# Optimization experiments

Measured on AMD Instinct MI355X. Metric: run time of the kernel, lower is better.

The kernel has to match this reference:

```python
import jax, jax.numpy as jnp
import numpy as np

B = 4            # batch
L = 4096         # max_len
D_MODEL = 1024   # qkv_dim == out_features
H = 16           # num_heads
SEG = 64         # max_seg_len
HD = D_MODEL // H          # head_dim = 64
NSEG = L // SEG            # num segments = 64
NEG = -1e10


def setup_inputs() -> dict:
    key = jax.random.key(0)
    k0, k1, k2, k3, k4 = jax.random.split(key, 5)
    scale = 1.0 / np.sqrt(D_MODEL).astype(np.float32)
    x = jax.random.normal(k0, (B, L, D_MODEL), jnp.float32)
    wq = jax.random.normal(k1, (D_MODEL, H, HD), jnp.float32) * scale
    wk = jax.random.normal(k2, (D_MODEL, H, HD), jnp.float32) * scale
    wv = jax.random.normal(k3, (D_MODEL, H, HD), jnp.float32) * scale
    wo = jax.random.normal(k4, (H, HD, D_MODEL), jnp.float32) * scale
    return {"input_qkv": x, "wq": wq, "wk": wk, "wv": wv, "wo": wo}


def reference(input_qkv, wq, wk, wv, wo):
    inv_sqrt_hd = 1.0 / np.sqrt(HD).astype(np.float32)
    # QKV projections; query pre-scaled by 1/sqrt(head_dim) as in get_qkv
    q = jnp.einsum('bld,dhf->blhf', input_qkv, wq) * inv_sqrt_hd
    k = jnp.einsum('bld,dhf->blhf', input_qkv, wk)
    v = jnp.einsum('bld,dhf->blhf', input_qkv, wv)

    cq = q.reshape(B * NSEG, SEG, H, HD)
    ck = k.reshape(B * NSEG, SEG, H, HD)
    cv = v.reshape(B * NSEG, SEG, H, HD)

    # Pooled per-segment query attends over its own segment's keys/values.
    # Original: merged_query = max(cq)*sqrt(HD), then flax dot_product_attention
    # rescales by 1/sqrt(HD) -> the two scalings cancel, so use max(cq) directly.
    mq = jnp.max(cq, axis=1, keepdims=True)                    # [B*NSEG, 1, H, HD]
    s_logits = jnp.einsum('bqhd,bkhd->bhqk', mq, ck)
    s_w = jax.nn.softmax(s_logits, axis=-1)
    s = jnp.einsum('bhqk,bkhd->bqhd', s_w, cv)                  # [B*NSEG, 1, H, HD]
    span_val = s.reshape(B, NSEG, H, HD)
    span_key = jnp.max(ck, axis=1).reshape(B, NSEG, H, HD)

    # Local causal attention logits within each segment
    causal = jnp.tril(jnp.ones((SEG, SEG), bool))
    local_bias = jnp.where(causal, 0.0, NEG).astype(jnp.float32)[None, :, None, :]
    local_logits = jnp.einsum('bqhd,bkhd->bqhk', cq, ck) + local_bias
    local_logits = local_logits.reshape(B, L, H, SEG)

    # Cross-segment logits: each token attends to strictly earlier segment summaries
    seg_id = jnp.arange(NSEG)
    prev_bias = jnp.where(seg_id[:, None] > seg_id[None, :], 0.0, NEG).astype(jnp.float32)
    prev_bias = jnp.repeat(prev_bias, SEG, axis=0)[None, :, None, :]  # [1, L, 1, NSEG]
    prev_logits = jnp.einsum('bqhd,bkhd->bqhk', q, span_key) + prev_bias

    # Joint softmax over [local keys | previous-segment summaries]
    joint = jnp.concatenate([local_logits, prev_logits], axis=-1)   # [B, L, H, SEG+NSEG]
    w = jax.nn.softmax(joint, axis=-1)
    local_att = w[..., :SEG].reshape(B * NSEG, SEG, H, SEG)
    prev_att = w[..., SEG:]

    local_merged = jnp.einsum('bqhk,bkhd->bqhd', local_att, cv).reshape(B, L, H, HD)
    prev_merged = jnp.einsum('bqhk,bkhd->bqhd', prev_att, span_val)

    return jnp.einsum('blhd,hdf->blf', local_merged + prev_merged, wo)
```

## Files before the change

kernel.cpp:

```cpp
#include <hip/hip_runtime.h>

#define BB    4
#define LL    4096
#define DM    1024
#define HH    16
#define SEGC  64
#define HDC   64
#define NSEGC 64
#define NEGV  -1.0e10f

typedef __bf16 bf16x8 __attribute__((ext_vector_type(8)));
typedef float  f32x4  __attribute__((ext_vector_type(4)));

__device__ __forceinline__ float bf2f(unsigned short s) {
  union { unsigned int u; float f; } x; x.u = ((unsigned int)s) << 16; return x.f;
}
__device__ __forceinline__ unsigned short f2bf(float f) {
  union { float f; unsigned int u; } x; x.f = f;
  unsigned int u = x.u;
  return (unsigned short)((u + 0x7fffu + ((u >> 16) & 1u)) >> 16);
}

__device__ __forceinline__ void gl2lds16(const unsigned short* g, unsigned short* l) {
  __builtin_amdgcn_global_load_lds(
      (const __attribute__((address_space(1))) unsigned int*)g,
      (__attribute__((address_space(3))) unsigned int*)l,
      16, 0, 0);
}

__device__ __forceinline__ void g2lds16(unsigned short* dst, const unsigned short* src) {
  int4 a = *(const int4*)(src);
  int4 b = *(const int4*)(src + 8);
  unsigned int* d = (unsigned int*)dst;
  const unsigned int* pa = (const unsigned int*)&a;
  const unsigned int* pb = (const unsigned int*)&b;
  d[0]=pa[0]; d[1]=pa[1]; d[2]=pa[2]; d[3]=pa[3];
  d[4]=pb[0]; d[5]=pb[1]; d[6]=pb[2]; d[7]=pb[3];
}

__global__ __launch_bounds__(256) void cvt_x(const float* __restrict__ x,
                                             unsigned short* __restrict__ xb) {
  const size_t i = ((size_t)blockIdx.x * 256 + threadIdx.x) * 8;
  float4 a = *(const float4*)(x + i);
  float4 b = *(const float4*)(x + i + 4);
  unsigned short o[8];
  o[0]=f2bf(a.x); o[1]=f2bf(a.y); o[2]=f2bf(a.z); o[3]=f2bf(a.w);
  o[4]=f2bf(b.x); o[5]=f2bf(b.y); o[6]=f2bf(b.z); o[7]=f2bf(b.w);
  *(int4*)(xb + i) = *(const int4*)o;
}

__global__ __launch_bounds__(256) void transpose_w(
    const float* __restrict__ wq, const float* __restrict__ wk,
    const float* __restrict__ wv, const float* __restrict__ wo,
    unsigned short* __restrict__ WqkvT, unsigned short* __restrict__ woT) {
  __shared__ unsigned short TS[64 * 65];

  const int z  = blockIdx.z;
  const int bx = blockIdx.x;
  const int by = blockIdx.y;
  const int t  = threadIdx.x;

  const float* src; unsigned short* dst; float scale = 1.0f;
  if (z == 0)      { src = wq; dst = WqkvT;               scale = 0.125f; }
  else if (z == 1) { src = wk; dst = WqkvT + 1024 * 1024; }
  else if (z == 2) { src = wv; dst = WqkvT + 2048 * 1024; }
  else             { src = wo; dst = woT; }

  const int rr = t >> 4;
  const int c4 = (t & 15) * 4;
  #pragma unroll
  for (int it = 0; it < 4; it++) {
    const int r = it * 16 + rr;
    float4 f = *(const float4*)(src + (size_t)(by * 64 + r) * 1024 + bx * 64 + c4);
    TS[(c4 + 0) * 65 + r] = f2bf(f.x * scale);
    TS[(c4 + 1) * 65 + r] = f2bf(f.y * scale);
    TS[(c4 + 2) * 65 + r] = f2bf(f.z * scale);
    TS[(c4 + 3) * 65 + r] = f2bf(f.w * scale);
  }
  __syncthreads();

  const int wr = t >> 3;
  const int w8 = (t & 7) * 8;
  #pragma unroll
  for (int it = 0; it < 2; it++) {
    const int n = it * 32 + wr;
    unsigned short o[8];
    #pragma unroll
    for (int j = 0; j < 8; j++) o[j] = TS[n * 65 + w8 + j];
    *(int4*)(dst + (size_t)(bx * 64 + n) * 1024 + by * 64 + w8) = *(const int4*)o;
  }
}

template <bool C_F32>
__global__ __launch_bounds__(512, 2) void gemm256(
    const unsigned short* __restrict__ A,
    const unsigned short* __restrict__ Bt,
    void* __restrict__ Cv,
    int ldc)
{
  __shared__ __align__(16) unsigned short L[2][2][4][4096];

  const int t    = threadIdx.x;
  const int wave = t >> 6;
  const int lane = t & 63;
  const int l15  = lane & 15;
  const int q4   = lane >> 4;
  const int wm   = wave >> 2;
  const int wn   = wave & 3;

  const int nwg = gridDim.x;
  const int wg  = blockIdx.x;
  const int swz = (wg & 7) * (nwg >> 3) + (wg >> 3);
  const int m0  = (swz & 63) << 8;
  const int n0  = (swz >> 6) << 8;

  const int srow = ((wave >> 1) << 4) + (lane >> 2);
  const int scol = ((wave & 1) << 5) + (((lane & 3) << 3) ^ (((lane >> 5) & 1) << 4));
  const size_t laneoff = (size_t)srow * 1024 + scol;
  const unsigned short* Ab = A  + (size_t)m0 * 1024 + laneoff;
  const unsigned short* Bb = Bt + (size_t)n0 * 1024 + laneoff;

  const int rdoff = l15 * 32 + ((q4 * 8) ^ (((l15 >> 3) & 1) << 4));

#define SA_(d, q, kt) gl2lds16(Ab + ((size_t)(q) * 64) * 1024 + (size_t)(kt) * 64, \
                               &L[d][0][q][0] + wave * 512)
#define SB_(d, q, kt) gl2lds16(Bb + ((size_t)(q) * 64) * 1024 + (size_t)(kt) * 64, \
                               &L[d][1][q][0] + wave * 512)
#define LDA8(d, i, kk) (*(const bf16x8*)(&L[d][0][wm * 2 + ((i) >> 2)][0] + \
                        ((((i) & 3) * 2 + (kk)) * 512) + rdoff))
#define LDB8(d, j, kk) (*(const bf16x8*)(&L[d][1][wn][0] + \
                        ((((j) * 2 + (kk))) * 512) + rdoff))
#define BAR()   asm volatile("s_barrier" ::: "memory")
#define LGKM0() asm volatile("s_waitcnt lgkmcnt(0)" ::: "memory")
#define VMW(n)  asm volatile("s_waitcnt vmcnt(" #n ")" ::: "memory")
#define MFMA_(av, bv, cv) __builtin_amdgcn_mfma_f32_16x16x32_bf16(av, bv, cv, 0, 0, 0)

  f32x4 acc[8][4];
  #pragma unroll
  for (int i = 0; i < 8; ++i)
    #pragma unroll
    for (int j = 0; j < 4; ++j) acc[i][j] = (f32x4){0.f, 0.f, 0.f, 0.f};

  SA_(0,0,0); SA_(0,2,0); SB_(0,0,0); SB_(0,1,0); SB_(0,2,0); SB_(0,3,0);
  SA_(0,1,0); SA_(0,3,0);
  SA_(1,0,1); SA_(1,2,1); SB_(1,0,1); SB_(1,1,1); SB_(1,2,1); SB_(1,3,1);
  VMW(6); BAR();

  #pragma unroll 1
  for (int it = 0; it < 8; ++it) {
    const int t1 = 2 * it + 1;
    const int t2 = (2 * it + 2) & 15;
    const int t3 = (2 * it + 3) & 15;
    bf16x8 a[4][2], b[4][2];

    #pragma unroll
    for (int ii = 0; ii < 4; ++ii) { a[ii][0] = LDA8(0, ii, 0); a[ii][1] = LDA8(0, ii, 1); }
    #pragma unroll
    for (int jj = 0; jj < 2; ++jj) { b[jj][0] = LDB8(0, jj, 0); b[jj][1] = LDB8(0, jj, 1); }
    SA_(1, 1, t1); SA_(1, 3, t1);
    BAR(); LGKM0();
    __builtin_amdgcn_s_setprio(1);
    #pragma unroll
    for (int ii = 0; ii < 4; ++ii)
      #pragma unroll
      for (int jj = 0; jj < 2; ++jj) {
        acc[ii][jj] = MFMA_(a[ii][0], b[jj][0], acc[ii][jj]);
        acc[ii][jj] = MFMA_(a[ii][1], b[jj][1], acc[ii][jj]);
      }
    __builtin_amdgcn_s_setprio(0);
    BAR();

    #pragma unroll
    for (int jj = 2; jj < 4; ++jj) { b[jj][0] = LDB8(0, jj, 0); b[jj][1] = LDB8(0, jj, 1); }
    SA_(0, 0, t2); SA_(0, 2, t2);
    BAR(); LGKM0();
    __builtin_amdgcn_s_setprio(1);
    #pragma unroll
    for (int ii = 0; ii < 4; ++ii)
      #pragma unroll
      for (int jj = 2; jj < 4; ++jj) {
        acc[ii][jj] = MFMA_(a[ii][0], b[jj][0], acc[ii][jj]);
        acc[ii][jj] = MFMA_(a[ii][1], b[jj][1], acc[ii][jj]);
      }
    __builtin_amdgcn_s_setprio(0);
    BAR();

    #pragma unroll
    for (int ii = 0; ii < 4; ++ii) { a[ii][0] = LDA8(0, 4 + ii, 0); a[ii][1] = LDA8(0, 4 + ii, 1); }
    SB_(0, 0, t2); SB_(0, 1, t2);
    BAR(); LGKM0();
    __builtin_amdgcn_s_setprio(1);
    #pragma unroll
    for (int ii = 0; ii < 4; ++ii)
      #pragma unroll
      for (int jj = 2; jj < 4; ++jj) {
        acc[4 + ii][jj] = MFMA_(a[ii][0], b[jj][0], acc[4 + ii][jj]);
        acc[4 + ii][jj] = MFMA_(a[ii][1], b[jj][1], acc[4 + ii][jj]);
      }
    __builtin_amdgcn_s_setprio(0);
    BAR();

    SB_(0, 2, t2); SB_(0, 3, t2);
    BAR();
    __builtin_amdgcn_s_setprio(1);
    #pragma unroll
    for (int ii = 0; ii < 4; ++ii)
      #pragma unroll
      for (int jj = 0; jj < 2; ++jj) {
        acc[4 + ii][jj] = MFMA_(a[ii][0], b[jj][0], acc[4 + ii][jj]);
        acc[4 + ii][jj] = MFMA_(a[ii][1], b[jj][1], acc[4 + ii][jj]);
      }
    __builtin_amdgcn_s_setprio(0);
    VMW(6); BAR();

    #pragma unroll
    for (int ii = 0; ii < 4; ++ii) { a[ii][0] = LDA8(1, ii, 0); a[ii][1] = LDA8(1, ii, 1); }
    #pragma unroll
    for (int jj = 0; jj < 2; ++jj) { b[jj][0] = LDB8(1, jj, 0); b[jj][1] = LDB8(1, jj, 1); }
    SA_(0, 1, t2); SA_(0, 3, t2);
    BAR(); LGKM0();
    __builtin_amdgcn_s_setprio(1);
    #pragma unroll
    for (int ii = 0; ii < 4; ++ii)
      #pragma unroll
      for (int jj = 0; jj < 2; ++jj) {
        acc[ii][jj] = MFMA_(a[ii][0], b[jj][0], acc[ii][jj]);
        acc[ii][jj] = MFMA_(a[ii][1], b[jj][1], acc[ii][jj]);
      }
    __builtin_amdgcn_s_setprio(0);
    BAR();

    #pragma unroll
    for (int jj = 2; jj < 4; ++jj) { b[jj][0] = LDB8(1, jj, 0); b[jj][1] = LDB8(1, jj, 1); }
    SA_(1, 0, t3); SA_(1, 2, t3);
    BAR(); LGKM0();
    __builtin_amdgcn_s_setprio(1);
    #pragma unroll
    for (int ii = 0; ii < 4; ++ii)
      #pragma unroll
      for (int jj = 2; jj < 4; ++jj) {
        acc[ii][jj] = MFMA_(a[ii][0], b[jj][0], acc[ii][jj]);
        acc[ii][jj] = MFMA_(a[ii][1], b[jj][1], acc[ii][jj]);
      }
    __builtin_amdgcn_s_setprio(0);
    BAR();

    #pragma unroll
    for (int ii = 0; ii < 4; ++ii) { a[ii][0] = LDA8(1, 4 + ii, 0); a[ii][1] = LDA8(1, 4 + ii, 1); }
    SB_(1, 0, t3); SB_(1, 1, t3);
    BAR(); LGKM0();
    __builtin_amdgcn_s_setprio(1);
    #pragma unroll
    for (int ii = 0; ii < 4; ++ii)
      #pragma unroll
      for (int jj = 2; jj < 4; ++jj) {
        acc[4 + ii][jj] = MFMA_(a[ii][0], b[jj][0], acc[4 + ii][jj]);
        acc[4 + ii][jj] = MFMA_(a[ii][1], b[jj][1], acc[4 + ii][jj]);
      }
    __builtin_amdgcn_s_setprio(0);
    BAR();

    SB_(1, 2, t3); SB_(1, 3, t3);
    BAR();
    __builtin_amdgcn_s_setprio(1);
    #pragma unroll
    for (int ii = 0; ii < 4; ++ii)
      #pragma unroll
      for (int jj = 0; jj < 2; ++jj) {
        acc[4 + ii][jj] = MFMA_(a[ii][0], b[jj][0], acc[4 + ii][jj]);
        acc[4 + ii][jj] = MFMA_(a[ii][1], b[jj][1], acc[4 + ii][jj]);
      }
    __builtin_amdgcn_s_setprio(0);
    VMW(6); BAR();
  }

  #pragma unroll
  for (int i = 0; i < 8; ++i) {
    #pragma unroll
    for (int j = 0; j < 4; ++j) {
      const int col = n0 + wn * 64 + j * 16 + l15;
      #pragma unroll
      for (int r = 0; r < 4; ++r) {
        const int row = m0 + wm * 128 + i * 16 + q4 * 4 + r;
        if (C_F32) ((float*)Cv)[(size_t)row * ldc + col] = acc[i][j][r];
        else ((unsigned short*)Cv)[(size_t)row * ldc + col] = f2bf(acc[i][j][r]);
      }
    }
  }
  VMW(0);

#undef SA_
#undef SB_
#undef LDA8
#undef LDB8
#undef BAR
#undef LGKM0
#undef VMW
#undef MFMA_
}

__global__ __launch_bounds__(64) void span_kernel(
    const unsigned short* __restrict__ qkv,
    unsigned short* __restrict__ spanK,
    unsigned short* __restrict__ spanV)
{
  __shared__ unsigned short QS[64 * 66], KS[64 * 66], VS[64 * 66];
  __shared__ float mqs[64], ws[64];

  const int c = blockIdx.x;
  const int h = blockIdx.y;
  const int b = c >> 6, n = c & 63;
  const int t = threadIdx.x;

  const size_t rowbase = ((size_t)(b * LL + n * SEGC + t)) * 3072 + h * 64;
  #pragma unroll
  for (int j = 0; j < 4; j++) {
    g2lds16(QS + t * 66 + j * 16, qkv + rowbase + j * 16);
    g2lds16(KS + t * 66 + j * 16, qkv + rowbase + 1024 + j * 16);
    g2lds16(VS + t * 66 + j * 16, qkv + rowbase + 2048 + j * 16);
  }
  __syncthreads();

  float mqa = -3.0e38f, mqb = -3.0e38f, ska = -3.0e38f, skc = -3.0e38f;
  #pragma unroll 8
  for (int r = 0; r < 64; r += 2) {
    mqa = fmaxf(mqa, bf2f(QS[r * 66 + t]));
    mqb = fmaxf(mqb, bf2f(QS[(r + 1) * 66 + t]));
    ska = fmaxf(ska, bf2f(KS[r * 66 + t]));
    skc = fmaxf(skc, bf2f(KS[(r + 1) * 66 + t]));
  }
  mqs[t] = fmaxf(mqa, mqb);
  spanK[((size_t)c * 16 + h) * 64 + t] = f2bf(fmaxf(ska, skc));
  __syncthreads();

  float l0 = 0.f, l1 = 0.f;
  #pragma unroll 8
  for (int d = 0; d < 64; d += 2) {
    l0 += mqs[d] * bf2f(KS[t * 66 + d]);
    l1 += mqs[d + 1] * bf2f(KS[t * 66 + d + 1]);
  }
  float logit = l0 + l1;
  float m = logit;
  #pragma unroll
  for (int off = 32; off; off >>= 1) m = fmaxf(m, __shfl_xor(m, off, 64));
  float e = __expf(logit - m);
  float s = e;
  #pragma unroll
  for (int off = 32; off; off >>= 1) s += __shfl_xor(s, off, 64);
  ws[t] = e / s;
  __syncthreads();

  float sv0 = 0.f, sv1 = 0.f;
  #pragma unroll 8
  for (int kk = 0; kk < 64; kk += 2) {
    sv0 += ws[kk] * bf2f(VS[kk * 66 + t]);
    sv1 += ws[kk + 1] * bf2f(VS[(kk + 1) * 66 + t]);
  }
  spanV[((size_t)c * 16 + h) * 64 + t] = f2bf(sv0 + sv1);
}

__global__ __launch_bounds__(256) void attn_kernel(
    const unsigned short* __restrict__ qkv,
    const unsigned short* __restrict__ spanK,
    const unsigned short* __restrict__ spanV,
    unsigned short* __restrict__ att)
{
  __shared__ unsigned short VT[64 * 136];
  __shared__ unsigned short WL[64 * 136];

  const int c = blockIdx.x;
  const int h = blockIdx.y;
  const int b = c >> 6, n = c & 63;
  const int t = threadIdx.x;
  const int wave = t >> 6;
  const int lane = t & 63;
  const int l15  = lane & 15;
  const int q4   = lane >> 4;

  #pragma unroll
  for (int it = 0; it < 4; it++) {
    const int idx = t + 256 * it;
    const int kp  = idx >> 3;
    const int fc  = (idx & 7) * 8;
    const unsigned short* src;
    if (kp < 64)
      src = qkv + ((size_t)(b * LL + n * SEGC + kp)) * 3072 + 2048 + h * 64 + fc;
    else
      src = spanV + ((size_t)(b * 64 + (kp - 64)) * 16 + h) * 64 + fc;
    int4 val = *(const int4*)src;
    const unsigned short* e = (const unsigned short*)&val;
    const int kb = kp >> 3;
    #pragma unroll
    for (int i = 0; i < 8; i++) {
      const int f  = fc + i;
      const int nb = (kb & 8) | ((kb ^ (f >> 3)) & 7);
      VT[f * 136 + nb * 8 + (kp & 7)] = e[i];
    }
  }

  bf16x8 af[2];
  {
    const size_t qbase = ((size_t)(b * LL + n * SEGC + wave * 16 + l15)) * 3072
                         + h * 64 + q4 * 8;
    af[0] = *(const bf16x8*)(qkv + qbase);
    af[1] = *(const bf16x8*)(qkv + qbase + 32);
  }

  f32x4 accl[8];
  #pragma unroll
  for (int tt = 0; tt < 8; tt++) accl[tt] = (f32x4){0.f, 0.f, 0.f, 0.f};

  #pragma unroll
  for (int s = 0; s < 2; s++) {
    bf16x8 bfr[8];
    #pragma unroll
    for (int tt = 0; tt < 8; tt++) {
      const unsigned short* src;
      if (tt < 4)
        src = qkv + ((size_t)(b * LL + n * SEGC + tt * 16 + l15)) * 3072
              + 1024 + h * 64 + s * 32 + q4 * 8;
      else
        src = spanK + ((size_t)((b * 64 + (tt - 4) * 16 + l15) * 16 + h)) * 64
              + s * 32 + q4 * 8;
      bfr[tt] = *(const bf16x8*)src;
    }
    #pragma unroll
    for (int tt = 0; tt < 8; tt++)
      accl[tt] = __builtin_amdgcn_mfma_f32_16x16x32_bf16(af[s], bfr[tt], accl[tt], 0, 0, 0);
  }

  #pragma unroll
  for (int tt = 0; tt < 8; tt++) {
    const int col = (tt & 3) * 16 + l15;
    #pragma unroll
    for (int rr = 0; rr < 4; rr++) {
      const int r_att = wave * 16 + q4 * 4 + rr;
      const bool valid = (tt < 4) ? (col <= r_att) : (col < n);
      if (!valid) accl[tt][rr] = NEGV;
    }
  }

  #pragma unroll
  for (int rr = 0; rr < 4; rr++) {
    float mx = accl[0][rr];
    #pragma unroll
    for (int tt = 1; tt < 8; tt++) mx = fmaxf(mx, accl[tt][rr]);
    #pragma unroll
    for (int msk = 1; msk < 16; msk <<= 1) mx = fmaxf(mx, __shfl_xor(mx, msk, 64));
    float sm = 0.f;
    float ex[8];
    #pragma unroll
    for (int tt = 0; tt < 8; tt++) { ex[tt] = __expf(accl[tt][rr] - mx); sm += ex[tt]; }
    #pragma unroll
    for (int msk = 1; msk < 16; msk <<= 1) sm += __shfl_xor(sm, msk, 64);
    const float inv = 1.0f / sm;
    const int r_att = wave * 16 + q4 * 4 + rr;
    #pragma unroll
    for (int tt = 0; tt < 8; tt++) {
      const int colj = (tt < 4) ? (tt * 16 + l15) : (64 + (tt - 4) * 16 + l15);
      WL[r_att * 136 + colj] = f2bf(ex[tt] * inv);
    }
  }

  __syncthreads();

  f32x4 accm[4];
  #pragma unroll
  for (int j = 0; j < 4; j++) accm[j] = (f32x4){0.f, 0.f, 0.f, 0.f};
  #pragma unroll
  for (int s = 0; s < 4; s++) {
    const bf16x8 aw = *(const bf16x8*)(WL + (wave * 16 + l15) * 136 + s * 32 + q4 * 8);
    #pragma unroll
    for (int j = 0; j < 4; j++) {
      const int f  = j * 16 + l15;
      const int kb = s * 4 + q4;
      const int nb = (kb & 8) | ((kb ^ (f >> 3)) & 7);
      const bf16x8 bv = *(const bf16x8*)(VT + f * 136 + nb * 8);
      accm[j] = __builtin_amdgcn_mfma_f32_16x16x32_bf16(aw, bv, accm[j], 0, 0, 0);
    }
  }

  #pragma unroll
  for (int j = 0; j < 4; j++) {
    #pragma unroll
    for (int rr = 0; rr < 4; rr++) {
      const int row = wave * 16 + q4 * 4 + rr;
      const int col = j * 16 + l15;
      att[((size_t)(b * LL + n * SEGC + row)) * 1024 + h * 64 + col] = f2bf(accm[j][rr]);
    }
  }
}

extern "C" void kernel_launch(void* const* d_in, const int* in_sizes, int n_in,
                              void* d_out, int out_size, void* d_ws, size_t ws_size,
                              hipStream_t stream) {
  const float* x  = (const float*)d_in[0];
  const float* wq = (const float*)d_in[1];
  const float* wk = (const float*)d_in[2];
  const float* wv = (const float*)d_in[3];
  const float* wo = (const float*)d_in[4];
  float* out = (float*)d_out;

  unsigned short* wsp   = (unsigned short*)d_ws;
  unsigned short* xb    = wsp;
  unsigned short* qkv   = xb + 16777216;
  unsigned short* WqkvT = qkv + 50331648;
  unsigned short* woT   = WqkvT + 3145728;
  unsigned short* skb   = woT + 1048576;
  unsigned short* svb   = skb + 262144;
  unsigned short* attb  = xb;

  cvt_x<<<8192, 256, 0, stream>>>(x, xb);
  transpose_w<<<dim3(16, 16, 4), 256, 0, stream>>>(wq, wk, wv, wo, WqkvT, woT);
  gemm256<false><<<768, 512, 0, stream>>>(xb, WqkvT, (void*)qkv, 3072);
  span_kernel<<<dim3(256, 16), 64, 0, stream>>>(qkv, skb, svb);
  attn_kernel<<<dim3(256, 16), 256, 0, stream>>>(qkv, skb, svb, attb);
  gemm256<true><<<256, 512, 0, stream>>>(attb, woT, (void*)out, 1024);
}
```

Before: 346.3 us.

## Software-pipeline LDS fragment reads with MFMA clusters in GEMM main loop

Restructures the GEMM inner loop so that LDS reads for the next MFMA cluster are issued before the current cluster runs, using separate register sets for the low/high A halves and for even/odd B fragments. Drops the explicit lgkmcnt(0) waits and extra barriers that previously serialized each LDS read phase against its MFMA phase. The prefetch of the next tile's A fragments moves to the end of the loop body, and the prologue issues one more load group. This raises register pressure through the extra fragment arrays and relies on compiler-inserted waits and sched_barrier for correctness.

```diff
diff --git a/kernel.cpp b/kernel.cpp
--- a/kernel.cpp
+++ b/kernel.cpp
@@ -131,9 +131,29 @@
 #define LDB8(d, j, kk) (*(const bf16x8*)(&L[d][1][wn][0] + \
                         ((((j) * 2 + (kk))) * 512) + rdoff))
 #define BAR()   asm volatile("s_barrier" ::: "memory")
-#define LGKM0() asm volatile("s_waitcnt lgkmcnt(0)" ::: "memory")
 #define VMW(n)  asm volatile("s_waitcnt vmcnt(" #n ")" ::: "memory")
 #define MFMA_(av, bv, cv) __builtin_amdgcn_mfma_f32_16x16x32_bf16(av, bv, cv, 0, 0, 0)
+
+  bf16x8 aLo[4][2], aHi[4][2], b01e[2][2], b01o[2][2], b23[2][2];
+
+#define RD_ALO(d) { _Pragma("unroll") for (int ii = 0; ii < 4; ++ii) { \
+    aLo[ii][0] = LDA8(d, ii, 0); aLo[ii][1] = LDA8(d, ii, 1); } }
+#define RD_AHI(d) { _Pragma("unroll") for (int ii = 0; ii < 4; ++ii) { \
+    aHi[ii][0] = LDA8(d, 4 + ii, 0); aHi[ii][1] = LDA8(d, 4 + ii, 1); } }
+#define RD_B01(d, ARR) { _Pragma("unroll") for (int jj = 0; jj < 2; ++jj) { \
+    ARR[jj][0] = LDB8(d, jj, 0); ARR[jj][1] = LDB8(d, jj, 1); } }
+#define RD_B23(d) { _Pragma("unroll") for (int jj = 0; jj < 2; ++jj) { \
+    b23[jj][0] = LDB8(d, 2 + jj, 0); b23[jj][1] = LDB8(d, 2 + jj, 1); } }
+
+#define CL(AR, BR, IO, J0) do { \
+    __builtin_amdgcn_sched_barrier(0); \
+    __builtin_amdgcn_s_setprio(1); \
+    _Pragma("unroll") for (int ii = 0; ii < 4; ++ii) { \
+      _Pragma("unroll") for (int jj = 0; jj < 2; ++jj) { \
+        acc[(IO) + ii][(J0) + jj] = MFMA_(AR[ii][0], BR[jj][0], acc[(IO) + ii][(J0) + jj]); \
+        acc[(IO) + ii][(J0) + jj] = MFMA_(AR[ii][1], BR[jj][1], acc[(IO) + ii][(J0) + jj]); \
+      } } \
+    __builtin_amdgcn_s_setprio(0); } while (0)
 
   f32x4 acc[8][4];
   #pragma unroll
@@ -144,134 +164,52 @@
   SA_(0,0,0); SA_(0,2,0); SB_(0,0,0); SB_(0,1,0); SB_(0,2,0); SB_(0,3,0);
   SA_(0,1,0); SA_(0,3,0);
   SA_(1,0,1); SA_(1,2,1); SB_(1,0,1); SB_(1,1,1); SB_(1,2,1); SB_(1,3,1);
-  VMW(6); BAR();
+  SA_(1,1,1); SA_(1,3,1);
+  VMW(8); BAR();
+  RD_ALO(0); RD_B01(0, b01e);
 
   #pragma unroll 1
   for (int it = 0; it < 8; ++it) {
-    const int t1 = 2 * it + 1;
     const int t2 = (2 * it + 2) & 15;
     const int t3 = (2 * it + 3) & 15;
-    bf16x8 a[4][2], b[4][2];
-
-    #pragma unroll
-    for (int ii = 0; ii < 4; ++ii) { a[ii][0] = LDA8(0, ii, 0); a[ii][1] = LDA8(0, ii, 1); }
-    #pragma unroll
-    for (int jj = 0; jj < 2; ++jj) { b[jj][0] = LDB8(0, jj, 0); b[jj][1] = LDB8(0, jj, 1); }
-    SA_(1, 1, t1); SA_(1, 3, t1);
-    BAR(); LGKM0();
-    __builtin_amdgcn_s_setprio(1);
-    #pragma unroll
-    for (int ii = 0; ii < 4; ++ii)
-      #pragma unroll
-      for (int jj = 0; jj < 2; ++jj) {
-        acc[ii][jj] = MFMA_(a[ii][0], b[jj][0], acc[ii][jj]);
-        acc[ii][jj] = MFMA_(a[ii][1], b[jj][1], acc[ii][jj]);
-      }
-    __builtin_amdgcn_s_setprio(0);
-    BAR();
-
-    #pragma unroll
-    for (int jj = 2; jj < 4; ++jj) { b[jj][0] = LDB8(0, jj, 0); b[jj][1] = LDB8(0, jj, 1); }
+
+    RD_B23(0);
     SA_(0, 0, t2); SA_(0, 2, t2);
-    BAR(); LGKM0();
-    __builtin_amdgcn_s_setprio(1);
-    #pragma unroll
-    for (int ii = 0; ii < 4; ++ii)
-      #pragma unroll
-      for (int jj = 2; jj < 4; ++jj) {
-        acc[ii][jj] = MFMA_(a[ii][0], b[jj][0], acc[ii][jj]);
-        acc[ii][jj] = MFMA_(a[ii][1], b[jj][1], acc[ii][jj]);
-      }
-    __builtin_amdgcn_s_setprio(0);
-    BAR();
-
-    #pragma unroll
-    for (int ii = 0; ii < 4; ++ii) { a[ii][0] = LDA8(0, 4 + ii, 0); a[ii][1] = LDA8(0, 4 + ii, 1); }
+    CL(aLo, b01e, 0, 0);
+    BAR();
+
+    RD_AHI(0);
     SB_(0, 0, t2); SB_(0, 1, t2);
-    BAR(); LGKM0();
-    __builtin_amdgcn_s_setprio(1);
-    #pragma unroll
-    for (int ii = 0; ii < 4; ++ii)
-      #pragma unroll
-      for (int jj = 2; jj < 4; ++jj) {
-        acc[4 + ii][jj] = MFMA_(a[ii][0], b[jj][0], acc[4 + ii][jj]);
-        acc[4 + ii][jj] = MFMA_(a[ii][1], b[jj][1], acc[4 + ii][jj]);
-      }
-    __builtin_amdgcn_s_setprio(0);
+    CL(aLo, b23, 0, 2);
     BAR();
 
     SB_(0, 2, t2); SB_(0, 3, t2);
-    BAR();
-    __builtin_amdgcn_s_setprio(1);
-    #pragma unroll
-    for (int ii = 0; ii < 4; ++ii)
-      #pragma unroll
-      for (int jj = 0; jj < 2; ++jj) {
-        acc[4 + ii][jj] = MFMA_(a[ii][0], b[jj][0], acc[4 + ii][jj]);
-        acc[4 + ii][jj] = MFMA_(a[ii][1], b[jj][1], acc[4 + ii][jj]);
-      }
-    __builtin_amdgcn_s_setprio(0);
+    CL(aHi, b23, 4, 2);
     VMW(6); BAR();
 
-    #pragma unroll
-    for (int ii = 0; ii < 4; ++ii) { a[ii][0] = LDA8(1, ii, 0); a[ii][1] = LDA8(1, ii, 1); }
-    #pragma unroll
-    for (int jj = 0; jj < 2; ++jj) { b[jj][0] = LDB8(1, jj, 0); b[jj][1] = LDB8(1, jj, 1); }
+    RD_ALO(1); RD_B01(1, b01o);
     SA_(0, 1, t2); SA_(0, 3, t2);
-    BAR(); LGKM0();
-    __builtin_amdgcn_s_setprio(1);
-    #pragma unroll
-    for (int ii = 0; ii < 4; ++ii)
-      #pragma unroll
-      for (int jj = 0; jj < 2; ++jj) {
-        acc[ii][jj] = MFMA_(a[ii][0], b[jj][0], acc[ii][jj]);
-        acc[ii][jj] = MFMA_(a[ii][1], b[jj][1], acc[ii][jj]);
-      }
-    __builtin_amdgcn_s_setprio(0);
-    BAR();
-
-    #pragma unroll
-    for (int jj = 2; jj < 4; ++jj) { b[jj][0] = LDB8(1, jj, 0); b[jj][1] = LDB8(1, jj, 1); }
+    CL(aHi, b01e, 4, 0);
+    BAR();
+
+    RD_B23(1);
     SA_(1, 0, t3); SA_(1, 2, t3);
-    BAR(); LGKM0();
-    __builtin_amdgcn_s_setprio(1);
-    #pragma unroll
-    for (int ii = 0; ii < 4; ++ii)
-      #pragma unroll
-      for (int jj = 2; jj < 4; ++jj) {
-        acc[ii][jj] = MFMA_(a[ii][0], b[jj][0], acc[ii][jj]);
-        acc[ii][jj] = MFMA_(a[ii][1], b[jj][1], acc[ii][jj]);
-      }
-    __builtin_amdgcn_s_setprio(0);
-    BAR();
-
-    #pragma unroll
-    for (int ii = 0; ii < 4; ++ii) { a[ii][0] = LDA8(1, 4 + ii, 0); a[ii][1] = LDA8(1, 4 + ii, 1); }
+    CL(aLo, b01o, 0, 0);
+    BAR();
+
+    RD_AHI(1);
     SB_(1, 0, t3); SB_(1, 1, t3);
-    BAR(); LGKM0();
-    __builtin_amdgcn_s_setprio(1);
-    #pragma unroll
-    for (int ii = 0; ii < 4; ++ii)
-      #pragma unroll
-      for (int jj = 2; jj < 4; ++jj) {
-        acc[4 + ii][jj] = MFMA_(a[ii][0], b[jj][0], acc[4 + ii][jj]);
-        acc[4 + ii][jj] = MFMA_(a[ii][1], b[jj][1], acc[4 + ii][jj]);
-      }
-    __builtin_amdgcn_s_setprio(0);
+    CL(aLo, b23, 0, 2);
     BAR();
 
     SB_(1, 2, t3); SB_(1, 3, t3);
-    BAR();
-    __builtin_amdgcn_s_setprio(1);
-    #pragma unroll
-    for (int ii = 0; ii < 4; ++ii)
-      #pragma unroll
-      for (int jj = 0; jj < 2; ++jj) {
-        acc[4 + ii][jj] = MFMA_(a[ii][0], b[jj][0], acc[4 + ii][jj]);
-        acc[4 + ii][jj] = MFMA_(a[ii][1], b[jj][1], acc[4 + ii][jj]);
-      }
-    __builtin_amdgcn_s_setprio(0);
+    CL(aHi, b23, 4, 2);
     VMW(6); BAR();
+
+    RD_ALO(0); RD_B01(0, b01e);
+    SA_(1, 1, t3); SA_(1, 3, t3);
+    CL(aHi, b01o, 4, 0);
+    BAR();
   }
 
   #pragma unroll
@@ -294,9 +232,13 @@
 #undef LDA8
 #undef LDB8
 #undef BAR
-#undef LGKM0
 #undef VMW
 #undef MFMA_
+#undef RD_ALO
+#undef RD_AHI
+#undef RD_B01
+#undef RD_B23
+#undef CL
 }
 
 __global__ __launch_bounds__(64) void span_kernel(
```

New measurement: 346.4 us. No clear change (+0.0%).

## Reorder GEMM prefetch schedule to load B first and stage attention keys in LDS

Applied to the files above, without the earlier changes.

The GEMM main loop's global-to-LDS prefetch order changes: B tiles are now issued before A tiles, all four B fragments are read from LDS at the first stage, and the vmcnt wait thresholds are adjusted to match. This is meant to drop one LDS read/barrier phase per half-iteration and give loads more time in flight. The attention kernel now stages the local keys and span keys into a padded LDS buffer with asynchronous global-to-LDS copies, instead of having each wave issue strided global loads for them. The cost is extra LDS use and an added block-wide barrier, and the changed wait counts must stay correct.

```diff
diff --git a/kernel.cpp b/kernel.cpp
--- a/kernel.cpp
+++ b/kernel.cpp
@@ -141,22 +141,22 @@
     #pragma unroll
     for (int j = 0; j < 4; ++j) acc[i][j] = (f32x4){0.f, 0.f, 0.f, 0.f};
 
-  SA_(0,0,0); SA_(0,2,0); SB_(0,0,0); SB_(0,1,0); SB_(0,2,0); SB_(0,3,0);
+  SB_(0,0,0); SB_(0,1,0); SB_(0,2,0); SB_(0,3,0); SA_(0,0,0); SA_(0,2,0);
   SA_(0,1,0); SA_(0,3,0);
-  SA_(1,0,1); SA_(1,2,1); SB_(1,0,1); SB_(1,1,1); SB_(1,2,1); SB_(1,3,1);
-  VMW(6); BAR();
+  SB_(1,0,1); SB_(1,1,1); SB_(1,2,1); SB_(1,3,1); SA_(1,0,1); SA_(1,2,1);
+  VMW(8); BAR();
 
   #pragma unroll 1
   for (int it = 0; it < 8; ++it) {
     const int t1 = 2 * it + 1;
-    const int t2 = (2 * it + 2) & 15;
-    const int t3 = (2 * it + 3) & 15;
+    const int s2 = (2 * it + 2) & 15;
+    const int s3 = (2 * it + 3) & 15;
     bf16x8 a[4][2], b[4][2];
 
     #pragma unroll
     for (int ii = 0; ii < 4; ++ii) { a[ii][0] = LDA8(0, ii, 0); a[ii][1] = LDA8(0, ii, 1); }
     #pragma unroll
-    for (int jj = 0; jj < 2; ++jj) { b[jj][0] = LDB8(0, jj, 0); b[jj][1] = LDB8(0, jj, 1); }
+    for (int jj = 0; jj < 4; ++jj) { b[jj][0] = LDB8(0, jj, 0); b[jj][1] = LDB8(0, jj, 1); }
     SA_(1, 1, t1); SA_(1, 3, t1);
     BAR(); LGKM0();
     __builtin_amdgcn_s_setprio(1);
@@ -170,10 +170,8 @@
     __builtin_amdgcn_s_setprio(0);
     BAR();
 
-    #pragma unroll
-    for (int jj = 2; jj < 4; ++jj) { b[jj][0] = LDB8(0, jj, 0); b[jj][1] = LDB8(0, jj, 1); }
-    SA_(0, 0, t2); SA_(0, 2, t2);
-    BAR(); LGKM0();
+    SB_(0, 0, s2); SB_(0, 1, s2);
+    BAR();
     __builtin_amdgcn_s_setprio(1);
     #pragma unroll
     for (int ii = 0; ii < 4; ++ii)
@@ -183,11 +181,11 @@
         acc[ii][jj] = MFMA_(a[ii][1], b[jj][1], acc[ii][jj]);
       }
     __builtin_amdgcn_s_setprio(0);
-    BAR();
+    VMW(10); BAR();
 
     #pragma unroll
     for (int ii = 0; ii < 4; ++ii) { a[ii][0] = LDA8(0, 4 + ii, 0); a[ii][1] = LDA8(0, 4 + ii, 1); }
-    SB_(0, 0, t2); SB_(0, 1, t2);
+    SB_(0, 2, s2); SB_(0, 3, s2);
     BAR(); LGKM0();
     __builtin_amdgcn_s_setprio(1);
     #pragma unroll
@@ -200,7 +198,7 @@
     __builtin_amdgcn_s_setprio(0);
     BAR();
 
-    SB_(0, 2, t2); SB_(0, 3, t2);
+    SA_(0, 0, s2); SA_(0, 2, s2);
     BAR();
     __builtin_amdgcn_s_setprio(1);
     #pragma unroll
@@ -211,13 +209,13 @@
         acc[4 + ii][jj] = MFMA_(a[ii][1], b[jj][1], acc[4 + ii][jj]);
       }
     __builtin_amdgcn_s_setprio(0);
-    VMW(6); BAR();
+    VMW(8); BAR();
 
     #pragma unroll
     for (int ii = 0; ii < 4; ++ii) { a[ii][0] = LDA8(1, ii, 0); a[ii][1] = LDA8(1, ii, 1); }
     #pragma unroll
-    for (int jj = 0; jj < 2; ++jj) { b[jj][0] = LDB8(1, jj, 0); b[jj][1] = LDB8(1, jj, 1); }
-    SA_(0, 1, t2); SA_(0, 3, t2);
+    for (int jj = 0; jj < 4; ++jj) { b[jj][0] = LDB8(1, jj, 0); b[jj][1] = LDB8(1, jj, 1); }
+    SA_(0, 1, s2); SA_(0, 3, s2);
     BAR(); LGKM0();
     __builtin_amdgcn_s_setprio(1);
     #pragma unroll
@@ -230,10 +228,8 @@
     __builtin_amdgcn_s_setprio(0);
     BAR();
 
-    #pragma unroll
-    for (int jj = 2; jj < 4; ++jj) { b[jj][0] = LDB8(1, jj, 0); b[jj][1] = LDB8(1, jj, 1); }
-    SA_(1, 0, t3); SA_(1, 2, t3);
-    BAR(); LGKM0();
+    SB_(1, 0, s3); SB_(1, 1, s3);
+    BAR();
     __builtin_amdgcn_s_setprio(1);
     #pragma unroll
     for (int ii = 0; ii < 4; ++ii)
@@ -243,11 +239,11 @@
         acc[ii][jj] = MFMA_(a[ii][1], b[jj][1], acc[ii][jj]);
       }
     __builtin_amdgcn_s_setprio(0);
-    BAR();
+    VMW(10); BAR();
 
     #pragma unroll
     for (int ii = 0; ii < 4; ++ii) { a[ii][0] = LDA8(1, 4 + ii, 0); a[ii][1] = LDA8(1, 4 + ii, 1); }
-    SB_(1, 0, t3); SB_(1, 1, t3);
+    SB_(1, 2, s3); SB_(1, 3, s3);
     BAR(); LGKM0();
     __builtin_amdgcn_s_setprio(1);
     #pragma unroll
@@ -260,7 +256,7 @@
     __builtin_amdgcn_s_setprio(0);
     BAR();
 
-    SB_(1, 2, t3); SB_(1, 3, t3);
+    SA_(1, 0, s3); SA_(1, 2, s3);
     BAR();
     __builtin_amdgcn_s_setprio(1);
     #pragma unroll
@@ -271,7 +267,7 @@
         acc[4 + ii][jj] = MFMA_(a[ii][1], b[jj][1], acc[4 + ii][jj]);
       }
     __builtin_amdgcn_s_setprio(0);
-    VMW(6); BAR();
+    VMW(8); BAR();
   }
 
   #pragma unroll
@@ -365,8 +361,9 @@
     const unsigned short* __restrict__ spanV,
     unsigned short* __restrict__ att)
 {
-  __shared__ unsigned short VT[64 * 136];
-  __shared__ unsigned short WL[64 * 136];
+  __shared__ __align__(16) unsigned short KJ[128 * 72];
+  __shared__ __align__(16) unsigned short VT[64 * 136];
+  __shared__ __align__(16) unsigned short WL[64 * 136];
 
   const int c = blockIdx.x;
   const int h = blockIdx.y;
@@ -376,6 +373,15 @@
   const int lane = t & 63;
   const int l15  = lane & 15;
   const int q4   = lane >> 4;
+
+  {
+    const int r  = t >> 2;
+    const int qq = (t & 3) * 16;
+    g2lds16(KJ + r * 72 + qq,
+            qkv + ((size_t)(b * LL + n * SEGC + r)) * 3072 + 1024 + h * 64 + qq);
+    g2lds16(KJ + (64 + r) * 72 + qq,
+            spanK + ((size_t)(b * 64 + r) * 16 + h) * 64 + qq);
+  }
 
   #pragma unroll
   for (int it = 0; it < 4; it++) {
@@ -406,6 +412,8 @@
     af[1] = *(const bf16x8*)(qkv + qbase + 32);
   }
 
+  __syncthreads();
+
   f32x4 accl[8];
   #pragma unroll
   for (int tt = 0; tt < 8; tt++) accl[tt] = (f32x4){0.f, 0.f, 0.f, 0.f};
@@ -414,16 +422,8 @@
   for (int s = 0; s < 2; s++) {
     bf16x8 bfr[8];
     #pragma unroll
-    for (int tt = 0; tt < 8; tt++) {
-      const unsigned short* src;
-      if (tt < 4)
-        src = qkv + ((size_t)(b * LL + n * SEGC + tt * 16 + l15)) * 3072
-              + 1024 + h * 64 + s * 32 + q4 * 8;
-      else
-        src = spanK + ((size_t)((b * 64 + (tt - 4) * 16 + l15) * 16 + h)) * 64
-              + s * 32 + q4 * 8;
-      bfr[tt] = *(const bf16x8*)src;
-    }
+    for (int tt = 0; tt < 8; tt++)
+      bfr[tt] = *(const bf16x8*)(KJ + (tt * 16 + l15) * 72 + s * 32 + q4 * 8);
     #pragma unroll
     for (int tt = 0; tt < 8; tt++)
       accl[tt] = __builtin_amdgcn_mfma_f32_16x16x32_bf16(af[s], bfr[tt], accl[tt], 0, 0, 0);
```

After: 328.0 us. 1.06x faster.
